# Kernel optimization log

Measured on AMD Instinct MI355X. Metric: run time of the kernel, lower is better.

The kernel has to match this reference:

```python
import jax, jax.numpy as jnp
import numpy as np

D_MODEL = 1024
NUM_HEADS = 16
D_KEY = 64
CTX = 2048
B, T = 2, 2048


def setup_inputs() -> dict:
    key = jax.random.key(0)
    ks = jax.random.split(key, 5)
    scale_in = 1.0 / np.sqrt(D_MODEL)
    scale_out = 1.0 / np.sqrt(NUM_HEADS * D_KEY)
    return {
        "X": jax.random.normal(ks[0], (B, T, D_MODEL), dtype=jnp.float32),
        "Wqkv": jax.random.uniform(ks[1], (D_MODEL, 3 * NUM_HEADS * D_KEY), dtype=jnp.float32, minval=-scale_in, maxval=scale_in),
        "bqkv": jax.random.uniform(ks[2], (3 * NUM_HEADS * D_KEY,), dtype=jnp.float32, minval=-scale_in, maxval=scale_in),
        "Wout": jax.random.uniform(ks[3], (NUM_HEADS * D_KEY, D_MODEL), dtype=jnp.float32, minval=-scale_out, maxval=scale_out),
        "bout": jax.random.uniform(ks[4], (D_MODEL,), dtype=jnp.float32, minval=-scale_out, maxval=scale_out),
    }


def reference(X, Wqkv, bqkv, Wout, bout):
    b, t, _ = X.shape
    # project and split into q, k, v: [B,T,3,H,Dk]
    qkv = (X @ Wqkv + bqkv).reshape(b, t, 3, NUM_HEADS, D_KEY)
    q = qkv[:, :, 0].transpose(0, 2, 1, 3)  # [B,H,T,Dk]
    k = qkv[:, :, 1].transpose(0, 2, 1, 3)
    v = qkv[:, :, 2].transpose(0, 2, 1, 3)
    scores = jnp.einsum("bhqd,bhkd->bhqk", q, k) / jnp.sqrt(jnp.float32(D_KEY))
    causal = jnp.tril(jnp.ones((t, t), dtype=bool))  # [T,T]
    scores = jnp.where(causal, scores, -jnp.inf)
    attn = jax.nn.softmax(scores, axis=-1)
    out = jnp.einsum("bhqk,bhkd->bhqd", attn, v)  # [B,H,T,Dk]
    out = out.transpose(0, 2, 1, 3).reshape(b, t, NUM_HEADS * D_KEY)
    return out @ Wout + bout
```

## Files before the change

kernel.cpp:

```cpp
#include <hip/hip_runtime.h>
#include <hip/hip_bf16.h>
#include <math.h>

static constexpr int Bc = 2, Hc = 16, Tc = 2048, DKc = 64, DMc = 1024, NQKV = 3072;
#define QSCALE 0.18033688011112042f

typedef unsigned short u16;
typedef unsigned int u32;
typedef short s8v __attribute__((ext_vector_type(8)));
typedef float f32x4 __attribute__((ext_vector_type(4)));
typedef float f32x16 __attribute__((ext_vector_type(16)));
typedef int i32x4 __attribute__((ext_vector_type(4)));

#define DEVINL __device__ __forceinline__

DEVINL u16 f2b(float f) {
    union { float f; unsigned u; } v; v.f = f;
    unsigned u = v.u;
    unsigned r = (u + 0x7fffu + ((u >> 16) & 1u)) >> 16;
    return (u16)r;
}

DEVINL u32 pkbf16(float lo, float up) {
    u32 r;
    asm volatile("v_cvt_pk_bf16_f32 %0, %1, %2" : "=v"(r) : "v"(lo), "v"(up));
    return r;
}

DEVINL float vexp2(float x) {
    float r;
    asm("v_exp_f32 %0, %1" : "=v"(r) : "v"(x));
    return r;
}

DEVINL void pl32swap(u32& a, u32& b) {
    asm volatile("v_permlane32_swap_b32 %0, %1" : "+v"(a), "+v"(b));
}

DEVINL void gl_lds(const void* g, void* l) {
    __builtin_amdgcn_global_load_lds(
        (const __attribute__((address_space(1))) unsigned int*)g,
        (__attribute__((address_space(3))) unsigned int*)l, 16, 0, 0);
}

DEVINL s8v as_s8v(i32x4 x) { union { i32x4 i; s8v v; } u; u.i = x; return u.v; }

__global__ __launch_bounds__(256) void conv_bf16(const float* __restrict__ in,
                                                 u16* __restrict__ outp, int n4) {
    int i = blockIdx.x * 256 + threadIdx.x;
    const int stride = gridDim.x * 256;
    for (; i < n4; i += stride) {
        float4 f = ((const float4*)in)[i];
        union { u16 u[4]; uint2 d; } o;
        o.u[0] = f2b(f.x); o.u[1] = f2b(f.y); o.u[2] = f2b(f.z); o.u[3] = f2b(f.w);
        ((uint2*)outp)[i] = o.d;
    }
}

__global__ __launch_bounds__(256) void transw(const float* __restrict__ W,
                                              u16* __restrict__ Wt, int N, int K) {
    __shared__ u16 LT[64][72];
    const int n0 = blockIdx.x * 64, k0 = blockIdx.y * 64;
    const int t = threadIdx.x;
    const int rr = t >> 4, cc = (t & 15) * 4;
    #pragma unroll
    for (int it = 0; it < 4; it++) {
        const int row = it * 16 + rr;
        float4 f = *(const float4*)&W[(size_t)(k0 + row) * N + n0 + cc];
        union { u16 u[4]; uint2 d; } o;
        o.u[0] = f2b(f.x); o.u[1] = f2b(f.y); o.u[2] = f2b(f.z); o.u[3] = f2b(f.w);
        *(uint2*)&LT[row][cc] = o.d;
    }
    __syncthreads();
    #pragma unroll
    for (int it = 0; it < 4; it++) {
        const int nrow = it * 16 + rr;
        union { u16 u[4]; uint2 d; } o;
        #pragma unroll
        for (int j = 0; j < 4; j++) o.u[j] = LT[cc + j][nrow];
        *(uint2*)&Wt[(size_t)(n0 + nrow) * K + k0 + cc] = o.d;
    }
}

template <int EPI>
__global__ __launch_bounds__(256) void gemm_bt(
    const u16* __restrict__ A, const u16* __restrict__ Bt,
    const float* __restrict__ bias,
    u16* __restrict__ q_out, u16* __restrict__ k_out, u16* __restrict__ v_out,
    float* __restrict__ f_out, int M, int N, int K, int ntn)
{
    __shared__ __align__(16) u16 Al[2][128 * 32];
    __shared__ __align__(16) u16 Bl[2][128 * 32];
    const int tid = threadIdx.x, lane = tid & 63, w = tid >> 6;
    const int qd = gridDim.x >> 3;
    const int wg = (blockIdx.x & 7) * qd + (blockIdx.x >> 3);
    const int m0 = (wg / ntn) * 128, n0 = (wg % ntn) * 128;
    const int wm = w >> 1, wn = w & 1;

    f32x4 acc[4][4] = {};

    const int arow = tid >> 2;
    const int acb = (tid & 3) * 16;
    const int nt = K >> 5;

#define GSTAGE(t_, b_) do {                                                    \
        const int kb_ = (t_) << 5;                                             \
        _Pragma("unroll")                                                      \
        for (int s_ = 0; s_ < 2; s_++) {                                       \
            const char* ga_ = (const char*)(A + (size_t)(m0 + s_ * 64 + arow) * K + kb_) + acb; \
            gl_lds(ga_, (char*)Al[b_] + s_ * 4096 + w * 1024);                 \
            const char* gb_ = (const char*)(Bt + (size_t)(n0 + s_ * 64 + arow) * K + kb_) + acb; \
            gl_lds(gb_, (char*)Bl[b_] + s_ * 4096 + w * 1024);                 \
        }                                                                      \
    } while (0)

    GSTAGE(0, 0);
    __syncthreads();
    int bufv = 0;
    for (int t = 0; t < nt; t++) {
        if (t + 1 < nt) GSTAGE(t + 1, bufv ^ 1);
        s8v af[4], bf[4];
        #pragma unroll
        for (int i = 0; i < 4; i++) {
            af[i] = *(const s8v*)((const char*)Al[bufv] + (wm * 64 + i * 16 + (lane & 15)) * 64 + (lane >> 4) * 16);
            bf[i] = *(const s8v*)((const char*)Bl[bufv] + (wn * 64 + i * 16 + (lane & 15)) * 64 + (lane >> 4) * 16);
        }
        #pragma unroll
        for (int mi = 0; mi < 4; mi++)
            #pragma unroll
            for (int ni = 0; ni < 4; ni++)
                acc[mi][ni] = __builtin_amdgcn_mfma_f32_16x16x32_bf16(af[mi], bf[ni], acc[mi][ni], 0, 0, 0);
        __syncthreads();
        bufv ^= 1;
    }
#undef GSTAGE

    #pragma unroll
    for (int mi = 0; mi < 4; mi++)
    #pragma unroll
    for (int ni = 0; ni < 4; ni++)
    #pragma unroll
    for (int r = 0; r < 4; r++) {
        const int row = m0 + wm * 64 + mi * 16 + (lane >> 4) * 4 + r;
        const int col = n0 + wn * 64 + ni * 16 + (lane & 15);
        const float val = acc[mi][ni][r] + bias[col];
        if constexpr (EPI == 0) {
            const int sel = col >> 10, rem = col & 1023;
            const int h = rem >> 6, d = rem & 63;
            const int b = row >> 11, t = row & 2047;
            const size_t idx = ((size_t)(b * Hc + h) * Tc + t) * DKc + d;
            if (sel == 0) q_out[idx] = f2b(val * QSCALE);
            else if (sel == 1) k_out[idx] = f2b(val);
            else v_out[idx] = f2b(val);
        } else {
            f_out[(size_t)row * N + col] = val;
        }
    }
}

__global__ __launch_bounds__(512) void attn_fwd(
    const u16* __restrict__ Q, const u16* __restrict__ K,
    const u16* __restrict__ V, u16* __restrict__ O)
{
    __shared__ __align__(16) char Gl[2][2][2][8192];

    const int bid = blockIdx.x;
    const int bh = bid & 31;
    const int qt = 15 - (bid >> 5);
    const int tid = threadIdx.x;
    const int g = tid >> 8;
    const int gtid = tid & 255;
    const int lane = tid & 63;
    const int ws = (tid >> 6) & 3;
    const int hi = lane >> 5, lq = lane & 31;
    const int q0w = qt * 128 + ws * 32;
    const int qg = q0w + lq;

    const u16* Qb = Q + (size_t)bh * (Tc * DKc);
    const u16* Kb = K + (size_t)bh * (Tc * DKc);
    const u16* Vb = V + (size_t)bh * (Tc * DKc);

    s8v qf[4];
    #pragma unroll
    for (int st = 0; st < 4; st++)
        qf[st] = *(const s8v*)(Qb + (size_t)qg * 64 + st * 16 + hi * 8);

    f32x16 o0 = {}, o1 = {}, lacc = {};

    const int dtw = (q0w + 31) >> 6;
    const int h = qt + 1;
    const int t0 = g * h;

    char* const Kbase = &Gl[g][0][0][0];
    char* const Vbase = &Gl[g][1][0][0];

    const int d2 = (gtid & 31) * 2, kb8 = gtid >> 5;
    const unsigned vsw0 = ((unsigned)(d2 & 7)) << 4;
    const unsigned vsw1 = ((unsigned)((d2 + 1) & 7)) << 4;
    const unsigned ksw = ((unsigned)(lq & 7)) << 4;

    u32 vx[8];

#define ISSUE_K(kt_, dst_) do {                                              \
        const char* Ktile_ = (const char*)(Kb + (size_t)(kt_) * 4096);       \
        _Pragma("unroll")                                                    \
        for (int s_ = 0; s_ < 2; s_++) {                                     \
            const int o_ = s_ * 4096 + gtid * 16;                            \
            const int rk_ = o_ >> 7;                                         \
            const int cb_ = (o_ & 127) ^ ((rk_ & 7) << 4);                   \
            gl_lds(Ktile_ + rk_ * 128 + cb_, (dst_) + s_ * 4096 + ws * 1024); \
        }                                                                    \
    } while (0)

#define LOAD_V(kt_) do {                                                     \
        const u16* Vtile_ = Vb + (size_t)(kt_) * 4096;                       \
        _Pragma("unroll")                                                    \
        for (int i_ = 0; i_ < 8; i_++)                                       \
            vx[i_] = *(const u32*)(Vtile_ + (kb8 * 8 + i_) * 64 + d2);       \
    } while (0)

#define WRITE_V(dst_) do {                                                   \
        s8v v0_, v1_;                                                        \
        _Pragma("unroll")                                                    \
        for (int i_ = 0; i_ < 8; i_++) {                                     \
            v0_[i_] = (short)(vx[i_] & 0xffff);                              \
            v1_[i_] = (short)(vx[i_] >> 16);                                 \
        }                                                                    \
        *(s8v*)((dst_) + d2 * 128 + (((unsigned)(kb8 * 16)) ^ vsw0)) = v0_;  \
        *(s8v*)((dst_) + (d2 + 1) * 128 + (((unsigned)(kb8 * 16)) ^ vsw1)) = v1_; \
    } while (0)

    ISSUE_K(t0, Kbase);
    LOAD_V(t0);
    WRITE_V(Vbase);
    __syncthreads();

    int c = 0;
    for (int i = 0; i < h; i++) {
        const int tki = t0 + i;
        const bool pf_next = (i + 1 < h);
        if (pf_next) {
            ISSUE_K(tki + 1, Kbase + (c ^ 1) * 8192);
            LOAD_V(tki + 1);
        }

        if (tki <= dtw) {
            const char* Kc = Kbase + c * 8192;
            const char* Vc = Vbase + c * 8192;
            f32x16 s0v = {}, s1v = {};
            __builtin_amdgcn_s_setprio(1);
            #pragma unroll
            for (int st = 0; st < 4; st++) {
                const unsigned cbs = (unsigned)(st * 32 + hi * 16);
                s8v kf0 = *(const s8v*)(Kc + lq * 128 + (cbs ^ ksw));
                s8v kf1 = *(const s8v*)(Kc + (32 + lq) * 128 + (cbs ^ ksw));
                s0v = __builtin_amdgcn_mfma_f32_32x32x16_bf16(kf0, qf[st], s0v, 0, 0, 0);
                s1v = __builtin_amdgcn_mfma_f32_32x32x16_bf16(kf1, qf[st], s1v, 0, 0, 0);
            }
            __builtin_amdgcn_s_setprio(0);

            if (tki == dtw) {
                #pragma unroll
                for (int r = 0; r < 16; r++) {
                    const int kg = tki * 64 + (r & 3) + 8 * (r >> 2) + 4 * hi;
                    if (kg > qg) s0v[r] = -INFINITY;
                    if (kg + 32 > qg) s1v[r] = -INFINITY;
                }
            }

            #pragma unroll
            for (int r = 0; r < 16; r++) {
                s0v[r] = vexp2(s0v[r]);
                s1v[r] = vexp2(s1v[r]);
            }
            lacc += s0v;
            lacc += s1v;

            i32x4 pf[4];
            #pragma unroll
            for (int gq = 0; gq < 2; gq++) {
                #pragma unroll
                for (int hq = 0; hq < 2; hq++) {
                    const int base = hq * 8;
                    u32 a0, a1, b0, b1;
                    if (gq == 0) {
                        a0 = pkbf16(s0v[base + 0], s0v[base + 1]);
                        a1 = pkbf16(s0v[base + 2], s0v[base + 3]);
                        b0 = pkbf16(s0v[base + 4], s0v[base + 5]);
                        b1 = pkbf16(s0v[base + 6], s0v[base + 7]);
                    } else {
                        a0 = pkbf16(s1v[base + 0], s1v[base + 1]);
                        a1 = pkbf16(s1v[base + 2], s1v[base + 3]);
                        b0 = pkbf16(s1v[base + 4], s1v[base + 5]);
                        b1 = pkbf16(s1v[base + 6], s1v[base + 7]);
                    }
                    pl32swap(a0, b0);
                    pl32swap(a1, b1);
                    pf[gq * 2 + hq][0] = (int)a0;
                    pf[gq * 2 + hq][1] = (int)a1;
                    pf[gq * 2 + hq][2] = (int)b0;
                    pf[gq * 2 + hq][3] = (int)b1;
                }
            }

            __builtin_amdgcn_s_setprio(1);
            #pragma unroll
            for (int ks = 0; ks < 4; ks++) {
                const unsigned cbv = (unsigned)(ks * 32 + hi * 16);
                s8v vf0 = *(const s8v*)(Vc + lq * 128 + (cbv ^ ksw));
                s8v vf1 = *(const s8v*)(Vc + (32 + lq) * 128 + (cbv ^ ksw));
                const s8v pa = as_s8v(pf[ks]);
                o0 = __builtin_amdgcn_mfma_f32_32x32x16_bf16(pa, vf0, o0, 0, 0, 0);
                o1 = __builtin_amdgcn_mfma_f32_32x32x16_bf16(pa, vf1, o1, 0, 0, 0);
            }
            __builtin_amdgcn_s_setprio(0);
        }

        if (pf_next) WRITE_V(Vbase + (c ^ 1) * 8192);
        __syncthreads();
        c ^= 1;
    }

    float t8[8];
    #pragma unroll
    for (int r = 0; r < 8; r++) t8[r] = lacc[r] + lacc[r + 8];
    #pragma unroll
    for (int off = 4; off >= 1; off >>= 1)
        #pragma unroll
        for (int r = 0; r < off; r++) t8[r] = t8[r] + t8[r + off];
    float ls = t8[0] + __shfl_xor(t8[0], 32);

    float* Pf = (float*)(&Gl[0][0][0][0]) + ws * 2304;
    if (g == 1) {
        float* dst = Pf + lane * 34;
        #pragma unroll
        for (int r = 0; r < 16; r++) { dst[r] = o0[r]; dst[16 + r] = o1[r]; }
        Pf[2176 + lane] = ls;
    }
    __syncthreads();
    if (g == 0) {
        const float* src = Pf + lane * 34;
        #pragma unroll
        for (int r = 0; r < 16; r++) { o0[r] += src[r]; o1[r] += src[16 + r]; }
        ls += Pf[2176 + lane];

        const float linv = 1.0f / ls;
        const int b = bh >> 4, hh = bh & 15;
        u16* Ob = O + ((size_t)b * Tc) * DMc + hh * 64;
        #pragma unroll
        for (int r = 0; r < 16; r++) {
            const int cr = (r & 3) + 8 * (r >> 2) + 4 * hi;
            const float ir = __shfl(linv, cr);
            u16* orow = Ob + (size_t)(q0w + cr) * DMc;
            orow[lq]      = f2b(o0[r] * ir);
            orow[32 + lq] = f2b(o1[r] * ir);
        }
    }
#undef ISSUE_K
#undef LOAD_V
#undef WRITE_V
}

extern "C" void kernel_launch(void* const* d_in, const int* in_sizes, int n_in,
                              void* d_out, int out_size, void* d_ws, size_t ws_size,
                              hipStream_t stream)
{
    const float* X    = (const float*)d_in[0];
    const float* Wqkv = (const float*)d_in[1];
    const float* bqkv = (const float*)d_in[2];
    const float* Wout = (const float*)d_in[3];
    const float* bout = (const float*)d_in[4];
    float* out = (float*)d_out;

    char* ws = (char*)d_ws;
    u16* Xb  = (u16*)(ws);
    u16* Ow  = (u16*)(ws);
    u16* Wt1 = (u16*)(ws + (8 << 20));
    u16* Wt2 = (u16*)(ws + (14 << 20));
    u16* Qw  = (u16*)(ws + (16 << 20));
    u16* Kw  = (u16*)(ws + (24 << 20));
    u16* Vw  = (u16*)(ws + (32 << 20));

    conv_bf16<<<2048, 256, 0, stream>>>(X, Xb, (Bc * Tc * DMc) / 4);
    transw<<<dim3(NQKV / 64, DMc / 64), 256, 0, stream>>>(Wqkv, Wt1, NQKV, DMc);
    transw<<<dim3(DMc / 64, DMc / 64), 256, 0, stream>>>(Wout, Wt2, DMc, DMc);

    gemm_bt<0><<<(Bc * Tc / 128) * (NQKV / 128), 256, 0, stream>>>(
        Xb, Wt1, bqkv, Qw, Kw, Vw, nullptr, Bc * Tc, NQKV, DMc, NQKV / 128);

    attn_fwd<<<512, 512, 0, stream>>>(Qw, Kw, Vw, Ow);

    gemm_bt<1><<<(Bc * Tc / 128) * (DMc / 128), 256, 0, stream>>>(
        Ow, Wt2, bout, nullptr, nullptr, nullptr, out, Bc * Tc, DMc, DMc, DMc / 128);
}
```

Baseline: 106.7 us.

## Triple-buffer GEMM K-loop with partial vmcnt waits and larger QKV tiles

The GEMM kernel is templated on the warp grid and per-warp tile counts. It now keeps three LDS stages in flight, prefetching two tiles ahead, and waits with a partial vmcnt plus a single barrier in place of a full wait and two syncs per step. The QKV projection switches to 256x256 tiles with 512 threads, giving 192 blocks. The aim is to hide global-load latency and reuse more data per tile, at the cost of more LDS and registers and fewer blocks to fill the CUs.

```diff
diff --git a/kernel.cpp b/kernel.cpp
--- a/kernel.cpp
+++ b/kernel.cpp
@@ -82,73 +82,89 @@
     }
 }
 
-template <int EPI>
-__global__ __launch_bounds__(256) void gemm_bt(
+template <int WM, int WN, int MI, int NI, int EPI>
+__global__ __launch_bounds__(WM * WN * 64) void gemm_pipe(
     const u16* __restrict__ A, const u16* __restrict__ Bt,
     const float* __restrict__ bias,
     u16* __restrict__ q_out, u16* __restrict__ k_out, u16* __restrict__ v_out,
     float* __restrict__ f_out, int M, int N, int K, int ntn)
 {
-    __shared__ __align__(16) u16 Al[2][128 * 32];
-    __shared__ __align__(16) u16 Bl[2][128 * 32];
+    constexpr int TH = WM * WN * 64;
+    constexpr int BM = WM * MI * 16;
+    constexpr int BN = WN * NI * 16;
+    __shared__ __align__(16) u16 Al[3][BM * 32];
+    __shared__ __align__(16) u16 Bl[3][BN * 32];
     const int tid = threadIdx.x, lane = tid & 63, w = tid >> 6;
     const int qd = gridDim.x >> 3;
     const int wg = (blockIdx.x & 7) * qd + (blockIdx.x >> 3);
-    const int m0 = (wg / ntn) * 128, n0 = (wg % ntn) * 128;
-    const int wm = w >> 1, wn = w & 1;
-
-    f32x4 acc[4][4] = {};
-
-    const int arow = tid >> 2;
-    const int acb = (tid & 3) * 16;
+    const int m0 = (wg / ntn) * BM, n0 = (wg % ntn) * BN;
+    const int wm = w / WN, wn = w % WN;
+
+    f32x4 acc[MI][NI] = {};
     const int nt = K >> 5;
 
-#define GSTAGE(t_, b_) do {                                                    \
-        const int kb_ = (t_) << 5;                                             \
+    char* pa0 = (char*)&Al[0][0]; char* pa1 = (char*)&Al[1][0]; char* pa2 = (char*)&Al[2][0];
+    char* pb0 = (char*)&Bl[0][0]; char* pb1 = (char*)&Bl[1][0]; char* pb2 = (char*)&Bl[2][0];
+
+    const int srow = tid >> 2;
+    const int scb  = (tid & 3) * 16;
+
+#define STG(t_, ad_, bd_) do {                                                 \
+        const int kk_ = (t_) << 5;                                             \
         _Pragma("unroll")                                                      \
         for (int s_ = 0; s_ < 2; s_++) {                                       \
-            const char* ga_ = (const char*)(A + (size_t)(m0 + s_ * 64 + arow) * K + kb_) + acb; \
-            gl_lds(ga_, (char*)Al[b_] + s_ * 4096 + w * 1024);                 \
-            const char* gb_ = (const char*)(Bt + (size_t)(n0 + s_ * 64 + arow) * K + kb_) + acb; \
-            gl_lds(gb_, (char*)Bl[b_] + s_ * 4096 + w * 1024);                 \
+            gl_lds((const char*)(A + (size_t)(m0 + s_ * (TH / 4) + srow) * K + kk_) + scb, \
+                   (ad_) + s_ * (TH * 16) + w * 1024);                         \
+            gl_lds((const char*)(Bt + (size_t)(n0 + s_ * (TH / 4) + srow) * K + kk_) + scb, \
+                   (bd_) + s_ * (TH * 16) + w * 1024);                         \
         }                                                                      \
     } while (0)
 
-    GSTAGE(0, 0);
-    __syncthreads();
-    int bufv = 0;
-    for (int t = 0; t < nt; t++) {
-        if (t + 1 < nt) GSTAGE(t + 1, bufv ^ 1);
-        s8v af[4], bf[4];
-        #pragma unroll
-        for (int i = 0; i < 4; i++) {
-            af[i] = *(const s8v*)((const char*)Al[bufv] + (wm * 64 + i * 16 + (lane & 15)) * 64 + (lane >> 4) * 16);
-            bf[i] = *(const s8v*)((const char*)Bl[bufv] + (wn * 64 + i * 16 + (lane & 15)) * 64 + (lane >> 4) * 16);
-        }
-        #pragma unroll
-        for (int mi = 0; mi < 4; mi++)
+    STG(0, pa0, pb0);
+    STG(1, pa1, pb1);
+
+    for (int t = 0; t < nt; ++t) {
+        if (t + 1 < nt) { asm volatile("s_waitcnt vmcnt(4)" ::: "memory"); }
+        else            { asm volatile("s_waitcnt vmcnt(0)" ::: "memory"); }
+        __builtin_amdgcn_sched_barrier(0);
+        __builtin_amdgcn_s_barrier();
+        __builtin_amdgcn_sched_barrier(0);
+
+        if (t + 2 < nt) STG(t + 2, pa2, pb2);
+
+        s8v af[MI], bf[NI];
+        #pragma unroll
+        for (int mi = 0; mi < MI; mi++)
+            af[mi] = *(const s8v*)(pa0 + (wm * (MI * 16) + mi * 16 + (lane & 15)) * 64 + (lane >> 4) * 16);
+        #pragma unroll
+        for (int ni = 0; ni < NI; ni++)
+            bf[ni] = *(const s8v*)(pb0 + (wn * (NI * 16) + ni * 16 + (lane & 15)) * 64 + (lane >> 4) * 16);
+        #pragma unroll
+        for (int mi = 0; mi < MI; mi++)
             #pragma unroll
-            for (int ni = 0; ni < 4; ni++)
+            for (int ni = 0; ni < NI; ni++)
                 acc[mi][ni] = __builtin_amdgcn_mfma_f32_16x16x32_bf16(af[mi], bf[ni], acc[mi][ni], 0, 0, 0);
-        __syncthreads();
-        bufv ^= 1;
-    }
-#undef GSTAGE
-
-    #pragma unroll
-    for (int mi = 0; mi < 4; mi++)
-    #pragma unroll
-    for (int ni = 0; ni < 4; ni++)
+
+        char* t_;
+        t_ = pa0; pa0 = pa1; pa1 = pa2; pa2 = t_;
+        t_ = pb0; pb0 = pb1; pb1 = pb2; pb2 = t_;
+    }
+#undef STG
+
+    #pragma unroll
+    for (int mi = 0; mi < MI; mi++)
+    #pragma unroll
+    for (int ni = 0; ni < NI; ni++)
     #pragma unroll
     for (int r = 0; r < 4; r++) {
-        const int row = m0 + wm * 64 + mi * 16 + (lane >> 4) * 4 + r;
-        const int col = n0 + wn * 64 + ni * 16 + (lane & 15);
+        const int row = m0 + wm * (MI * 16) + mi * 16 + (lane >> 4) * 4 + r;
+        const int col = n0 + wn * (NI * 16) + ni * 16 + (lane & 15);
         const float val = acc[mi][ni][r] + bias[col];
         if constexpr (EPI == 0) {
             const int sel = col >> 10, rem = col & 1023;
             const int h = rem >> 6, d = rem & 63;
-            const int b = row >> 11, t = row & 2047;
-            const size_t idx = ((size_t)(b * Hc + h) * Tc + t) * DKc + d;
+            const int b = row >> 11, tt = row & 2047;
+            const size_t idx = ((size_t)(b * Hc + h) * Tc + tt) * DKc + d;
             if (sel == 0) q_out[idx] = f2b(val * QSCALE);
             else if (sel == 1) k_out[idx] = f2b(val);
             else v_out[idx] = f2b(val);
@@ -385,11 +401,11 @@
     transw<<<dim3(NQKV / 64, DMc / 64), 256, 0, stream>>>(Wqkv, Wt1, NQKV, DMc);
     transw<<<dim3(DMc / 64, DMc / 64), 256, 0, stream>>>(Wout, Wt2, DMc, DMc);
 
-    gemm_bt<0><<<(Bc * Tc / 128) * (NQKV / 128), 256, 0, stream>>>(
-        Xb, Wt1, bqkv, Qw, Kw, Vw, nullptr, Bc * Tc, NQKV, DMc, NQKV / 128);
+    gemm_pipe<2, 4, 8, 4, 0><<<192, 512, 0, stream>>>(
+        Xb, Wt1, bqkv, Qw, Kw, Vw, nullptr, Bc * Tc, NQKV, DMc, NQKV / 256);
 
     attn_fwd<<<512, 512, 0, stream>>>(Qw, Kw, Vw, Ow);
 
-    gemm_bt<1><<<(Bc * Tc / 128) * (DMc / 128), 256, 0, stream>>>(
+    gemm_pipe<2, 2, 4, 4, 1><<<256, 256, 0, stream>>>(
         Ow, Wt2, bout, nullptr, nullptr, nullptr, out, Bc * Tc, DMc, DMc, DMc / 128);
 }
```

Result: slower. 125.1 us (+17.2%).
